# Kernel optimization log

Hardware: AMD Instinct MI355X
Metric: run time of the kernel (lower is better)

## Reference

```python
import jax, jax.numpy as jnp
import numpy as np

N, D_FEAT, HIDDEN, HEADS, NUM_CLASSES = 6000, 512, 256, 8, 32
NEG_INF = -1e9
LEAKY_ALPHA = 0.2


def gat_head(x, adj_bias, W, a1, a2):
    """Single dense GAT attention head (NSL GraphAttnLayer, inference mode).

    x: [N, D], W: [D, F], a1/a2: [F]. Returns [N, F].
    """
    h = x @ W                       # [N, F]
    f1 = h @ a1                     # [N] source term
    f2 = h @ a2                     # [N] destination term
    e = jax.nn.leaky_relu(f1[:, None] + f2[None, :], LEAKY_ALPHA) + adj_bias
    coefs = jax.nn.softmax(e, axis=-1)  # softmax over neighbors j
    return coefs @ h                # [N, F]


def setup_inputs() -> dict:
    key = jax.random.key(0)
    ks = jax.random.split(key, 8)
    features = jax.random.normal(ks[0], (N, D_FEAT), dtype=jnp.float32)
    adj = jax.random.randint(ks[1], (N, N), 0, 2, dtype=jnp.int32)
    # Block 0: 8 heads, each D_FEAT -> HIDDEN
    W0 = jax.random.normal(ks[2], (HEADS, D_FEAT, HIDDEN), dtype=jnp.float32) / np.sqrt(D_FEAT)
    a10 = jax.random.normal(ks[3], (HEADS, HIDDEN), dtype=jnp.float32) / np.sqrt(HIDDEN)
    a20 = jax.random.normal(ks[4], (HEADS, HIDDEN), dtype=jnp.float32) / np.sqrt(HIDDEN)
    # Classifier: single head, HEADS*HIDDEN -> NUM_CLASSES
    Wc = jax.random.normal(ks[5], (HEADS * HIDDEN, NUM_CLASSES), dtype=jnp.float32) / np.sqrt(HEADS * HIDDEN)
    a1c = jax.random.normal(ks[6], (NUM_CLASSES,), dtype=jnp.float32) / np.sqrt(NUM_CLASSES)
    a2c = jax.random.normal(ks[7], (NUM_CLASSES,), dtype=jnp.float32) / np.sqrt(NUM_CLASSES)
    return {"features": features, "adj": adj, "W0": W0, "a10": a10,
            "a20": a20, "Wc": Wc, "a1c": a1c, "a2c": a2c}


def reference(features, adj, W0, a10, a20, Wc, a1c, a2c):
    adj_bias = jnp.where(adj > 0, 0.0, NEG_INF).astype(jnp.float32)  # [N, N]
    # GATBlock: 8 heads concatenated, then ELU (dropout is identity at inference)
    heads = [gat_head(features, adj_bias, W0[h], a10[h], a20[h]) for h in range(HEADS)]
    x = jax.nn.elu(jnp.concatenate(heads, axis=1))  # [N, HEADS*HIDDEN]
    # Classifier GraphAttnLayer -> [N, NUM_CLASSES]
    return gat_head(x, adj_bias, Wc, a1c, a2c)
```

## Files before the change

kernel.cpp:

```cpp
#include <hip/hip_runtime.h>
#include <hip/hip_bf16.h>

#define NN 6000
#define NPAD 6016
#define DF 512
#define HID 256
#define NH 8
#define NC 32
#define FTOT 2048
#define MSTR 96
#define NJB (NPAD / 64)
#define NJT (NPAD / 32)
#define L2E 1.4426950408889634f

using short8 = __attribute__((ext_vector_type(8))) short;
using f32x16 = __attribute__((ext_vector_type(16))) float;
using f32x4  = __attribute__((ext_vector_type(4))) float;

__device__ __forceinline__ unsigned short f2bf(float f) {
    unsigned int u = __float_as_uint(f);
    return (unsigned short)((u + 0x7fffu + ((u >> 16) & 1u)) >> 16);
}
__device__ __forceinline__ float bf2f(unsigned short s) {
    return __uint_as_float(((unsigned int)s) << 16);
}
__device__ __forceinline__ void gl16(const void* g, void* l) {
    __builtin_amdgcn_global_load_lds(
        (const __attribute__((address_space(1))) unsigned int*)g,
        (__attribute__((address_space(3))) unsigned int*)l, 16, 0, 0);
}


__global__ void pack_bits(const int* __restrict__ adj, unsigned char* __restrict__ maskb) {
    int row = blockIdx.y;
    int b = blockIdx.x * 256 + threadIdx.x;
    if (b >= 768) return;
    int j0 = b * 8;
    unsigned int v = 0;
    if (j0 + 7 < NN) {
        const int4* p = (const int4*)(adj + (size_t)row * NN + j0);
        int4 a = p[0], c = p[1];
        v = (unsigned)((a.x>0) | ((a.y>0)<<1) | ((a.z>0)<<2) | ((a.w>0)<<3)
          | ((c.x>0)<<4) | ((c.y>0)<<5) | ((c.z>0)<<6) | ((c.w>0)<<7));
    }
    maskb[(size_t)row * 768 + b] = (unsigned char)v;
}

__global__ void cast_x4(const float* __restrict__ x, unsigned short* __restrict__ xb, int n4) {
    int i = blockIdx.x * 256 + threadIdx.x;
    if (i >= n4) return;
    float4 v = ((const float4*)x)[i];
    unsigned long long pk = (unsigned long long)f2bf(v.x)
        | ((unsigned long long)f2bf(v.y) << 16)
        | ((unsigned long long)f2bf(v.z) << 32)
        | ((unsigned long long)f2bf(v.w) << 48);
    ((unsigned long long*)xb)[i] = pk;
}

__global__ void wt_pack(const float* __restrict__ W0, unsigned short* __restrict__ Wt) {
    int fp = blockIdx.x;
    int h = fp >> 8, f = fp & 255;
    for (int k = threadIdx.x; k < DF; k += 256)
        Wt[(size_t)fp * DF + k] = f2bf(W0[(((size_t)h * DF + k) << 8) | f]);
}

__global__ void wct_pack(const float* __restrict__ Wc, unsigned short* __restrict__ Wct) {
    int c = blockIdx.x;
    for (int k = threadIdx.x; k < FTOT; k += 256)
        Wct[(size_t)c * FTOT + k] = f2bf(Wc[(size_t)k * NC + c]);
}

__global__ __launch_bounds__(256, 2) void gemm_h(const unsigned short* __restrict__ A,
                                                 const unsigned short* __restrict__ B,
                                                 unsigned short* __restrict__ Ht) {
    __shared__ __align__(16) unsigned short As[128 * 64];
    __shared__ __align__(16) unsigned short Bs[128 * 64];
    const int w = threadIdx.x >> 6, l = threadIdx.x & 63;
    const int lrow = l & 31, kh = l >> 5;
    const int wm = w >> 1, wn = w & 1;
    const int mbase = blockIdx.x * 128, nbase = blockIdx.y * 128;
    const int srcc = (l & 7) ^ (l >> 3);
    f32x16 acc[2][2];
#pragma unroll
    for (int i = 0; i < 2; ++i)
#pragma unroll
        for (int j = 0; j < 2; ++j) acc[i][j] = (f32x16)0.0f;

#pragma unroll 1
    for (int kb = 0; kb < DF / 64; ++kb) {
        __syncthreads();
#pragma unroll
        for (int q = 0; q < 4; ++q) {
            int c = q * 4 + w;
            int r = c * 8 + (l >> 3);
            int arow = mbase + r; if (arow > NN - 1) arow = NN - 1;
            gl16(A + (size_t)arow * DF + kb * 64 + srcc * 8, (char*)As + c * 1024);
            gl16(B + (size_t)(nbase + r) * DF + kb * 64 + srcc * 8, (char*)Bs + c * 1024);
        }
        __syncthreads();
#pragma unroll
        for (int kk = 0; kk < 4; ++kk) {
            short8 av[2], bv[2];
#pragma unroll
            for (int mt = 0; mt < 2; ++mt) {
                int r = wm * 64 + mt * 32 + lrow;
                av[mt] = *(const short8*)((const char*)As + r * 128 + ((((kk << 1) | kh) ^ (r & 7)) << 4));
            }
#pragma unroll
            for (int ft = 0; ft < 2; ++ft) {
                int r = wn * 64 + ft * 32 + lrow;
                bv[ft] = *(const short8*)((const char*)Bs + r * 128 + ((((kk << 1) | kh) ^ (r & 7)) << 4));
            }
#pragma unroll
            for (int mt = 0; mt < 2; ++mt)
#pragma unroll
                for (int ft = 0; ft < 2; ++ft)
                    acc[mt][ft] = __builtin_amdgcn_mfma_f32_32x32x16_bf16(av[mt], bv[ft], acc[mt][ft], 0, 0, 0);
        }
    }
#pragma unroll
    for (int mt = 0; mt < 2; ++mt)
#pragma unroll
        for (int ft = 0; ft < 2; ++ft) {
            size_t n = nbase + wn * 64 + ft * 32 + lrow;
#pragma unroll
            for (int g = 0; g < 4; ++g) {
                int m0 = mbase + wm * 64 + mt * 32 + (g << 3) + (kh << 2);
                unsigned long long pk =
                    (unsigned long long)f2bf(acc[mt][ft][g * 4 + 0]) |
                    ((unsigned long long)f2bf(acc[mt][ft][g * 4 + 1]) << 16) |
                    ((unsigned long long)f2bf(acc[mt][ft][g * 4 + 2]) << 32) |
                    ((unsigned long long)f2bf(acc[mt][ft][g * 4 + 3]) << 48);
                *(unsigned long long*)(Ht + n * NPAD + m0) = pk;
            }
        }
}

__global__ void f12_kern(const unsigned short* __restrict__ Ht, const float* __restrict__ a1,
                         const float* __restrict__ a2, float* __restrict__ f1, float* __restrict__ f2,
                         int fdim) {
    int h = blockIdx.y;
    int i = blockIdx.x * 256 + threadIdx.x;
    if (i >= NPAD) return;
    float s1 = 0.f, s2 = 0.f;
    const unsigned short* base = Ht + (size_t)h * fdim * NPAD + i;
    for (int f = 0; f < fdim; ++f) {
        float v = bf2f(base[(size_t)f * NPAD]);
        s1 = fmaf(v, a1[h * fdim + f], s1);
        s2 = fmaf(v, a2[h * fdim + f], s2);
    }
    f1[(size_t)h * NPAD + i] = s1 * L2E;
    f2[(size_t)h * NPAD + i] = s2 * L2E;
}

__global__ void rarb_kern(const float* __restrict__ f1all, const float* __restrict__ f2all,
                          float* __restrict__ RA, float* __restrict__ RB,
                          float* __restrict__ E2F, float* __restrict__ E2Fb) {
    int h = blockIdx.x;
    __shared__ float red[8];
    const float* f2h = f2all + (size_t)h * NPAD;
    float m = -3.0e38f;
    for (int i = threadIdx.x; i < NN; i += 256) m = fmaxf(m, f2h[i]);
    for (int off = 32; off; off >>= 1) m = fmaxf(m, __shfl_xor(m, off));
    if ((threadIdx.x & 63) == 0) red[threadIdx.x >> 6] = m;
    __syncthreads();
    if (threadIdx.x == 0)
        red[4] = fmaxf(fmaxf(red[0], red[1]), fmaxf(red[2], red[3]));
    __syncthreads();
    float Mh = red[4];
    for (int i = threadIdx.x; i < NPAD; i += 256) {
        float F1 = (i < NN) ? f1all[(size_t)h * NPAD + i] : 0.f;
        float t2 = F1 + Mh;
        float Mi = fmaxf(t2, 0.2f * t2);
        RA[(size_t)h * NPAD + i] = F1 - Mi;
        RB[(size_t)h * NPAD + i] = 0.2f * F1 - Mi;
        float v2 = f2h[i];
        E2F[(size_t)h * NPAD + i] = exp2f(v2);
        E2Fb[(size_t)h * NPAD + i] = exp2f(0.2f * v2);
    }
}

__global__ __launch_bounds__(256, 3) void attn_main(
    const unsigned short* __restrict__ Ht,
    const unsigned long long* __restrict__ mask,
    const float* __restrict__ RA, const float* __restrict__ RB,
    const float* __restrict__ E2F, const float* __restrict__ E2Fb,
    unsigned short* __restrict__ x2)
{
    __shared__ __align__(16) unsigned short htile[3 * 256 * 32];
    const int bid = blockIdx.x;
    const int h = bid & 7;
    const int rowbase = (bid >> 3) * 64;
    const int w = threadIdx.x >> 6, l = threadIdx.x & 63;
    const int la = l & 15;
    const int s  = l >> 4;
    const int rowA = rowbase + w * 16 + la;
    const int rowAc = (rowA < NN) ? rowA : NN - 1;
    const unsigned short* Hh = Ht + (size_t)h * HID * NPAD;
    const float* E2Fh = E2F + (size_t)h * NPAD;
    const float* E2Fbh = E2Fb + (size_t)h * NPAD;
    const float era = exp2f(RA[(size_t)h * NPAD + rowAc]);
    const float erb = exp2f(RB[(size_t)h * NPAD + rowAc]);
    const short8 ones = { (short)0x3F80, (short)0x3F80, (short)0x3F80, (short)0x3F80,
                          (short)0x3F80, (short)0x3F80, (short)0x3F80, (short)0x3F80 };
    f32x4 acc16[16];
    f32x4 asum4 = (f32x4)0.0f;
#pragma unroll
    for (int i = 0; i < 16; ++i) acc16[i] = (f32x4)0.0f;

    const int segsrc = (l & 3) ^ ((l >> 3) & 3);
    auto STAGE = [&](int buf, int jt) {
#pragma unroll
        for (int q = 0; q < 4; ++q) {
            int c = q * 4 + w;
            int f = c * 16 + (l >> 2);
            gl16(Hh + (size_t)f * NPAD + jt * 32 + segsrc * 8,
                 (char*)htile + buf * 16384 + c * 1024);
        }
    };

    STAGE(0, 0);
#pragma unroll 1
    for (int jt = 0; jt < NJT; ++jt) {
        if (jt + 1 < NJT) STAGE((jt + 1) % 3, jt + 1);
        asm volatile("s_waitcnt vmcnt(4)" ::: "memory");
        __builtin_amdgcn_sched_barrier(0);
        __builtin_amdgcn_s_barrier();
        __builtin_amdgcn_sched_barrier(0);
        const char* tb = (const char*)htile + (jt % 3) * 16384;
        unsigned int mwrd = ((const unsigned int*)mask)[(size_t)rowAc * 192 + jt];
        unsigned int mbyte = (mwrd >> (s * 8)) & 0xffu;
        int j0 = jt * 32 + s * 8;
        f32x4 ea0 = *(const f32x4*)(E2Fh + j0);
        f32x4 ea1 = *(const f32x4*)(E2Fh + j0 + 4);
        f32x4 eb0 = *(const f32x4*)(E2Fbh + j0);
        f32x4 eb1 = *(const f32x4*)(E2Fbh + j0 + 4);
        float p[8];
#pragma unroll
        for (int e = 0; e < 8; ++e) {
            float fe = (e < 4) ? ea0[e & 3] : ea1[e & 3];
            float fb = (e < 4) ? eb0[e & 3] : eb1[e & 3];
            float pe = fmaxf(era * fe, erb * fb);
            p[e] = (mbyte & (1u << e)) ? pe : 0.f;
        }
        union { unsigned int u[4]; short8 s8; } cv;
#pragma unroll
        for (int q = 0; q < 4; ++q)
            cv.u[q] = __builtin_amdgcn_perm(__float_as_uint(p[2 * q + 1]),
                                            __float_as_uint(p[2 * q]), 0x07060302u);
        __builtin_amdgcn_s_setprio(1);
        asum4 = __builtin_amdgcn_mfma_f32_16x16x32_bf16(cv.s8, ones, asum4, 0, 0, 0);
#pragma unroll
        for (int ft = 0; ft < 16; ++ft) {
            int fl = ft * 16 + la;
            int slot = s ^ ((fl >> 1) & 3);
            short8 bfrag = *(const short8*)(tb + fl * 64 + slot * 16);
            acc16[ft] = __builtin_amdgcn_mfma_f32_16x16x32_bf16(cv.s8, bfrag, acc16[ft], 0, 0, 0);
        }
        __builtin_amdgcn_s_setprio(0);
    }

    float dinv[4];
#pragma unroll
    for (int t = 0; t < 4; ++t)
        dinv[t] = (asum4[t] > 0.f) ? (1.0f / asum4[t]) : 0.f;

#pragma unroll
    for (int ft = 0; ft < 16; ++ft)
#pragma unroll
        for (int t = 0; t < 4; ++t) {
            int grow = rowbase + w * 16 + s * 4 + t;
            if (grow < NN) {
                float v = acc16[ft][t] * dinv[t];
                v = (v > 0.f) ? v : (__expf(v) - 1.f);
                x2[(size_t)grow * FTOT + h * HID + ft * 16 + la] = f2bf(v);
            }
        }
}

__global__ __launch_bounds__(256, 2) void gemm_hc(const unsigned short* __restrict__ A,
                                                  const unsigned short* __restrict__ B,
                                                  float* __restrict__ pk) {
    int w = threadIdx.x >> 6, l = threadIdx.x & 63;
    int lrow = l & 31, kh = l >> 5;
    int q = blockIdx.y;
    int nbase = blockIdx.x * 128 + w * 32;
    int brow = nbase + lrow; if (brow > NN - 1) brow = NN - 1;
    f32x16 acc = (f32x16)0.0f;
    const short8* ap = (const short8*)(A + (size_t)lrow * FTOT + q * 256 + kh * 8);
    const short8* bp = (const short8*)(B + (size_t)brow * FTOT + q * 256 + kh * 8);
#pragma unroll
    for (int kk = 0; kk < 16; ++kk) {
        short8 af = ap[kk * 2];
        short8 bf = bp[kk * 2];
        acc = __builtin_amdgcn_mfma_f32_32x32x16_bf16(af, bf, acc, 0, 0, 0);
    }
    int i = nbase + lrow;
#pragma unroll
    for (int g = 0; g < 4; ++g) {
        int c0 = (g << 3) + (kh << 2);
#pragma unroll
        for (int r = 0; r < 4; ++r)
            pk[((size_t)q * NC + c0 + r) * NPAD + i] = acc[g * 4 + r];
    }
}

__global__ void merge_hc(const float* __restrict__ pk, unsigned short* __restrict__ hct) {
    int i = blockIdx.x * 256 + threadIdx.x;
    int c = blockIdx.y;
    if (i >= NPAD) return;
    float s = 0.f;
#pragma unroll
    for (int q = 0; q < 8; ++q) s += pk[((size_t)q * NC + c) * NPAD + i];
    hct[(size_t)c * NPAD + i] = f2bf(s);
}

__global__ __launch_bounds__(256) void cls_part(
    const unsigned short* __restrict__ hctb,
    const unsigned long long* __restrict__ mask,
    const float* __restrict__ RAc, const float* __restrict__ RBc,
    const float* __restrict__ E2Fc, const float* __restrict__ E2Fcb,
    float* __restrict__ pacc, float* __restrict__ pdsum)
{
    const int w = threadIdx.x >> 6, l = threadIdx.x & 63;
    const int lrow = l & 31, kh = l >> 5;
    const int q = blockIdx.y;
    const int rowbase = blockIdx.x * 128;
    const int myrow = rowbase + w * 32 + lrow;
    const bool act = myrow < NN;
    const float era = exp2f(RAc[myrow]);
    const float erb = exp2f(RBc[myrow]);
    const int JB0 = q * 12, JB1 = (JB0 + 12 < NJB) ? JB0 + 12 : NJB;
    const short8 ones = { (short)0x3F80, (short)0x3F80, (short)0x3F80, (short)0x3F80,
                          (short)0x3F80, (short)0x3F80, (short)0x3F80, (short)0x3F80 };
    f32x16 acc = (f32x16)0.0f;
    f32x16 asum = (f32x16)0.0f;

#pragma unroll 1
    for (int jb = JB0; jb < JB1; ++jb) {
        unsigned long long mword = act ? mask[(size_t)myrow * MSTR + jb] : 0ull;
#pragma unroll
        for (int kk = 0; kk < 4; ++kk) {
            short8 bfrag = *(const short8*)(hctb + (size_t)lrow * NPAD + jb * 64 + (kk * 2 + kh) * 8);
            unsigned int mbyte = (unsigned int)((mword >> (kk * 16 + kh * 8)) & 0xffull);
            int j0 = jb * 64 + kk * 16 + kh * 8;
            f32x4 ea0 = *(const f32x4*)(E2Fc + j0);
            f32x4 ea1 = *(const f32x4*)(E2Fc + j0 + 4);
            f32x4 eb0 = *(const f32x4*)(E2Fcb + j0);
            f32x4 eb1 = *(const f32x4*)(E2Fcb + j0 + 4);
            float p[8];
#pragma unroll
            for (int e = 0; e < 8; ++e) {
                float fe = (e < 4) ? ea0[e & 3] : ea1[e & 3];
                float fb = (e < 4) ? eb0[e & 3] : eb1[e & 3];
                float pe = fmaxf(era * fe, erb * fb);
                p[e] = (mbyte & (1u << e)) ? pe : 0.f;
            }
            union { unsigned int u[4]; short8 s8; } cv;
#pragma unroll
            for (int t = 0; t < 4; ++t)
                cv.u[t] = __builtin_amdgcn_perm(__float_as_uint(p[2 * t + 1]),
                                                __float_as_uint(p[2 * t]), 0x07060302u);
            asum = __builtin_amdgcn_mfma_f32_32x32x16_bf16(cv.s8, ones, asum, 0, 0, 0);
            acc = __builtin_amdgcn_mfma_f32_32x32x16_bf16(cv.s8, bfrag, acc, 0, 0, 0);
        }
    }
#pragma unroll
    for (int g = 0; g < 4; ++g)
#pragma unroll
        for (int rr = 0; rr < 4; ++rr) {
            int i = rowbase + w * 32 + (g << 3) + (kh << 2) + rr;
            pacc[((size_t)q * NPAD + i) * NC + lrow] = acc[g * 4 + rr];
            if (lrow == 0) pdsum[(size_t)q * NPAD + i] = asum[g * 4 + rr];
        }
}

__global__ void cls_merge(const float* __restrict__ pacc, const float* __restrict__ pdsum,
                          float* __restrict__ outp) {
    int i = blockIdx.x * 8 + (threadIdx.x >> 5);
    int c = threadIdx.x & 31;
    if (i >= NN) return;
    float num = 0.f, den = 0.f;
#pragma unroll
    for (int q = 0; q < 8; ++q) {
        num += pacc[((size_t)q * NPAD + i) * NC + c];
        den += pdsum[(size_t)q * NPAD + i];
    }
    outp[(size_t)i * NC + c] = (den > 0.f) ? num / den : 0.f;
}

extern "C" void kernel_launch(void* const* d_in, const int* in_sizes, int n_in,
                              void* d_out, int out_size, void* d_ws, size_t ws_size,
                              hipStream_t stream) {
    const float* features = (const float*)d_in[0];
    const int*   adj      = (const int*)d_in[1];
    const float* W0       = (const float*)d_in[2];
    const float* a10      = (const float*)d_in[3];
    const float* a20      = (const float*)d_in[4];
    const float* Wc       = (const float*)d_in[5];
    const float* a1c      = (const float*)d_in[6];
    const float* a2c      = (const float*)d_in[7];
    float* out = (float*)d_out;

    char* p = (char*)d_ws;
    auto alloc = [&](size_t bytes) { char* r = p; p += (bytes + 255) & ~(size_t)255; return r; };
    unsigned long long* mask = (unsigned long long*)alloc((size_t)NN * MSTR * 8);
    unsigned short* Xbf = (unsigned short*)alloc((size_t)NN * DF * 2);
    unsigned short* Wt  = (unsigned short*)alloc((size_t)FTOT * DF * 2);
    unsigned short* Ht  = (unsigned short*)alloc((size_t)FTOT * NPAD * 2);
    unsigned short* x2  = (unsigned short*)alloc((size_t)NN * FTOT * 2);
    unsigned short* Wct = (unsigned short*)alloc((size_t)NC * FTOT * 2);
    unsigned short* hct = (unsigned short*)alloc((size_t)NC * NPAD * 2);
    float* f1  = (float*)alloc((size_t)NH * NPAD * 4);
    float* f2  = (float*)alloc((size_t)NH * NPAD * 4);
    float* RA  = (float*)alloc((size_t)NH * NPAD * 4);
    float* RB  = (float*)alloc((size_t)NH * NPAD * 4);
    float* E2F  = (float*)alloc((size_t)NH * NPAD * 4);
    float* E2Fb = (float*)alloc((size_t)NH * NPAD * 4);
    float* f1c  = (float*)alloc((size_t)NPAD * 4);
    float* f2c  = (float*)alloc((size_t)NPAD * 4);
    float* RAc  = (float*)alloc((size_t)NPAD * 4);
    float* RBc  = (float*)alloc((size_t)NPAD * 4);
    float* E2Fc  = (float*)alloc((size_t)NPAD * 4);
    float* E2Fcb = (float*)alloc((size_t)NPAD * 4);
    float* pkhc  = (float*)Xbf;
    float* pacc  = (float*)Xbf;
    float* pdsum = pacc + (size_t)8 * NPAD * NC;

    pack_bits<<<dim3(3, NN), 256, 0, stream>>>(adj, (unsigned char*)mask);
    cast_x4<<<(NN * DF / 4 + 255) / 256, 256, 0, stream>>>(features, Xbf, NN * DF / 4);
    wt_pack<<<FTOT, 256, 0, stream>>>(W0, Wt);
    wct_pack<<<NC, 256, 0, stream>>>(Wc, Wct);

    gemm_h<<<dim3(NPAD / 128, FTOT / 128), 256, 0, stream>>>(Xbf, Wt, Ht);
    f12_kern<<<dim3((NPAD + 255) / 256, NH), 256, 0, stream>>>(Ht, a10, a20, f1, f2, HID);
    rarb_kern<<<NH, 256, 0, stream>>>(f1, f2, RA, RB, E2F, E2Fb);

    attn_main<<<dim3(94 * NH), 256, 0, stream>>>(Ht, mask, RA, RB, E2F, E2Fb, x2);

    gemm_hc<<<dim3(NPAD / 128, 8), 256, 0, stream>>>(Wct, x2, pkhc);
    merge_hc<<<dim3((NPAD + 255) / 256, NC), 256, 0, stream>>>(pkhc, hct);
    f12_kern<<<dim3((NPAD + 255) / 256, 1), 256, 0, stream>>>(hct, a1c, a2c, f1c, f2c, NC);
    rarb_kern<<<1, 256, 0, stream>>>(f1c, f2c, RAc, RBc, E2Fc, E2Fcb);

    cls_part<<<dim3(47, 8), 256, 0, stream>>>(hct, mask, RAc, RBc, E2Fc, E2Fcb, pacc, pdsum);
    cls_merge<<<750, 256, 0, stream>>>(pacc, pdsum, out);
}
```

Baseline: 430.1 us.

## Fuse classifier projection into attention epilogue, dropping x2 round-trip

The attention kernel now writes its ELU output tile into shared memory and multiplies it directly by the per-head slice of the classifier weights with MFMA. It emits per-head partial classifier projections instead of the full bf16 x2 activation matrix. The separate gemm_hc kernel is removed, and a new merge kernel sums the 8 head partials. This cuts a large global write and re-read of the N×2048 intermediate plus one launch. In exchange the attention epilogue gets longer, adds a barrier and global reads of Wct per wave.

```diff
diff --git a/kernel.cpp b/kernel.cpp
--- a/kernel.cpp
+++ b/kernel.cpp
@@ -185,7 +185,8 @@
     const unsigned long long* __restrict__ mask,
     const float* __restrict__ RA, const float* __restrict__ RB,
     const float* __restrict__ E2F, const float* __restrict__ E2Fb,
-    unsigned short* __restrict__ x2)
+    const unsigned short* __restrict__ Wct,
+    float* __restrict__ hcp)
 {
     __shared__ __align__(16) unsigned short htile[3 * 256 * 32];
     const int bid = blockIdx.x;
@@ -265,54 +266,48 @@
     for (int t = 0; t < 4; ++t)
         dinv[t] = (asum4[t] > 0.f) ? (1.0f / asum4[t]) : 0.f;
 
+    __syncthreads();
+    unsigned short* vlds = htile + w * 4096;
 #pragma unroll
     for (int ft = 0; ft < 16; ++ft)
 #pragma unroll
         for (int t = 0; t < 4; ++t) {
-            int grow = rowbase + w * 16 + s * 4 + t;
-            if (grow < NN) {
-                float v = acc16[ft][t] * dinv[t];
-                v = (v > 0.f) ? v : (__expf(v) - 1.f);
-                x2[(size_t)grow * FTOT + h * HID + ft * 16 + la] = f2bf(v);
-            }
-        }
-}
-
-__global__ __launch_bounds__(256, 2) void gemm_hc(const unsigned short* __restrict__ A,
-                                                  const unsigned short* __restrict__ B,
-                                                  float* __restrict__ pk) {
-    int w = threadIdx.x >> 6, l = threadIdx.x & 63;
-    int lrow = l & 31, kh = l >> 5;
-    int q = blockIdx.y;
-    int nbase = blockIdx.x * 128 + w * 32;
-    int brow = nbase + lrow; if (brow > NN - 1) brow = NN - 1;
-    f32x16 acc = (f32x16)0.0f;
-    const short8* ap = (const short8*)(A + (size_t)lrow * FTOT + q * 256 + kh * 8);
-    const short8* bp = (const short8*)(B + (size_t)brow * FTOT + q * 256 + kh * 8);
-#pragma unroll
-    for (int kk = 0; kk < 16; ++kk) {
-        short8 af = ap[kk * 2];
-        short8 bf = bp[kk * 2];
-        acc = __builtin_amdgcn_mfma_f32_32x32x16_bf16(af, bf, acc, 0, 0, 0);
-    }
-    int i = nbase + lrow;
-#pragma unroll
-    for (int g = 0; g < 4; ++g) {
-        int c0 = (g << 3) + (kh << 2);
-#pragma unroll
-        for (int r = 0; r < 4; ++r)
-            pk[((size_t)q * NC + c0 + r) * NPAD + i] = acc[g * 4 + r];
-    }
-}
-
-__global__ void merge_hc(const float* __restrict__ pk, unsigned short* __restrict__ hct) {
-    int i = blockIdx.x * 256 + threadIdx.x;
-    int c = blockIdx.y;
+            int r = s * 4 + t;
+            float v = acc16[ft][t] * dinv[t];
+            v = (v > 0.f) ? v : (__expf(v) - 1.f);
+            int f = ft * 16 + la;
+            int byt = r * 512 + ((f * 2) ^ ((r & 7) << 4));
+            *(unsigned short*)((char*)vlds + byt) = f2bf(v);
+        }
+    f32x4 cacc0 = (f32x4)0.0f, cacc1 = (f32x4)0.0f;
+#pragma unroll
+    for (int kk = 0; kk < 8; ++kk) {
+        short8 afrag = *(const short8*)((char*)vlds + la * 512 + ((kk * 64 + s * 16) ^ ((la & 7) << 4)));
+        short8 b0 = *(const short8*)(Wct + (size_t)la * FTOT + h * HID + kk * 32 + s * 8);
+        short8 b1 = *(const short8*)(Wct + (size_t)(16 + la) * FTOT + h * HID + kk * 32 + s * 8);
+        cacc0 = __builtin_amdgcn_mfma_f32_16x16x32_bf16(afrag, b0, cacc0, 0, 0, 0);
+        cacc1 = __builtin_amdgcn_mfma_f32_16x16x32_bf16(afrag, b1, cacc1, 0, 0, 0);
+    }
+#pragma unroll
+    for (int t = 0; t < 4; ++t) {
+        int grow = rowbase + w * 16 + s * 4 + t;
+        if (grow < NN) {
+            hcp[((size_t)h * NPAD + grow) * NC + la] = cacc0[t];
+            hcp[((size_t)h * NPAD + grow) * NC + 16 + la] = cacc1[t];
+        }
+    }
+}
+
+__global__ void merge_hcp(const float* __restrict__ hcp, unsigned short* __restrict__ hct) {
+    int idx = blockIdx.x * 256 + threadIdx.x;
+    int i = idx >> 5, c = idx & 31;
     if (i >= NPAD) return;
-    float s = 0.f;
-#pragma unroll
-    for (int q = 0; q < 8; ++q) s += pk[((size_t)q * NC + c) * NPAD + i];
-    hct[(size_t)c * NPAD + i] = f2bf(s);
+    float sum = 0.f;
+    if (i < NN) {
+#pragma unroll
+        for (int hh = 0; hh < NH; ++hh) sum += hcp[((size_t)hh * NPAD + i) * NC + c];
+    }
+    hct[(size_t)c * NPAD + i] = f2bf(sum);
 }
 
 __global__ __launch_bounds__(256) void cls_part(
@@ -408,7 +403,6 @@
     unsigned short* Xbf = (unsigned short*)alloc((size_t)NN * DF * 2);
     unsigned short* Wt  = (unsigned short*)alloc((size_t)FTOT * DF * 2);
     unsigned short* Ht  = (unsigned short*)alloc((size_t)FTOT * NPAD * 2);
-    unsigned short* x2  = (unsigned short*)alloc((size_t)NN * FTOT * 2);
     unsigned short* Wct = (unsigned short*)alloc((size_t)NC * FTOT * 2);
     unsigned short* hct = (unsigned short*)alloc((size_t)NC * NPAD * 2);
     float* f1  = (float*)alloc((size_t)NH * NPAD * 4);
@@ -423,7 +417,7 @@
     float* RBc  = (float*)alloc((size_t)NPAD * 4);
     float* E2Fc  = (float*)alloc((size_t)NPAD * 4);
     float* E2Fcb = (float*)alloc((size_t)NPAD * 4);
-    float* pkhc  = (float*)Xbf;
+    float* hcp   = (float*)Xbf;
     float* pacc  = (float*)Xbf;
     float* pdsum = pacc + (size_t)8 * NPAD * NC;
 
@@ -436,10 +430,9 @@
     f12_kern<<<dim3((NPAD + 255) / 256, NH), 256, 0, stream>>>(Ht, a10, a20, f1, f2, HID);
     rarb_kern<<<NH, 256, 0, stream>>>(f1, f2, RA, RB, E2F, E2Fb);
 
-    attn_main<<<dim3(94 * NH), 256, 0, stream>>>(Ht, mask, RA, RB, E2F, E2Fb, x2);
-
-    gemm_hc<<<dim3(NPAD / 128, 8), 256, 0, stream>>>(Wct, x2, pkhc);
-    merge_hc<<<dim3((NPAD + 255) / 256, NC), 256, 0, stream>>>(pkhc, hct);
+    attn_main<<<dim3(94 * NH), 256, 0, stream>>>(Ht, mask, RA, RB, E2F, E2Fb, Wct, hcp);
+
+    merge_hcp<<<(NPAD * NC + 255) / 256, 256, 0, stream>>>(hcp, hct);
     f12_kern<<<dim3((NPAD + 255) / 256, 1), 256, 0, stream>>>(hct, a1c, a2c, f1c, f2c, NC);
     rarb_kern<<<1, 256, 0, stream>>>(f1c, f2c, RAc, RBc, E2Fc, E2Fcb);
 
```

Measured after the change: 418.4 us. -2.7%, faster.
